# Optimization experiments

Hardware: AMD Instinct MI355X
Metric: run time of the kernel (lower is better)

Reference implementation:

```python
import jax, jax.numpy as jnp
import numpy as np

H, N, M, F, D = 8, 4096, 4096, 1024, 256

def setup_inputs() -> dict:
    key = jax.random.key(0)
    ks = jax.random.split(key, 8)
    sc = 0.02
    return {
        "this": jax.random.normal(ks[0], (N, F), dtype=jnp.float32),
        "that": jax.random.normal(ks[1], (M, F), dtype=jnp.float32),
        "mask": jax.random.randint(ks[2], (N, M), 0, 2) > 0,
        "Wq": jax.random.normal(ks[3], (H, F, D), dtype=jnp.float32) * sc,
        "bq": jnp.zeros((H, D), dtype=jnp.float32),
        "Wk": jax.random.normal(ks[4], (H, F, D), dtype=jnp.float32) * sc,
        "bk": jnp.zeros((H, D), dtype=jnp.float32),
        "Wv": jax.random.normal(ks[5], (H, F, D), dtype=jnp.float32) * sc,
        "bv": jnp.zeros((H, D), dtype=jnp.float32),
        "Wo": jax.random.normal(ks[6], (2 * F, F), dtype=jnp.float32) * sc,
        "bo": jnp.zeros((F,), dtype=jnp.float32),
    }

def reference(this, that, mask, Wq, bq, Wk, bk, Wv, bv, Wo, bo):
    # Per-head projections, batched over heads. q:[h,n,d] k,v:[h,m,d]
    q = jnp.einsum('nf,hfd->hnd', this, Wq) + bq[:, None, :]
    k = jnp.einsum('mf,hfd->hmd', that, Wk) + bk[:, None, :]
    v = jnp.einsum('mf,hfd->hmd', that, Wv) + bv[:, None, :]
    # Unscaled attention scores [h,n,m]
    s = jnp.einsum('hnd,hmd->hnm', q, k)
    neg = 1e9 * (~mask).astype(s.dtype)              # additive mask [n,m]
    head_ids = jnp.arange(s.shape[0])[:, None, None]  # mask applies to heads >= 4 only
    s = jnp.where(head_ids >= 4, s - neg, s)
    w = jax.nn.softmax(s, axis=-1)
    r = jnp.einsum('hnm,hmd->hnd', w, v)              # [h,n,d]
    # concat heads along feature axis in head order -> [n, h*d]
    cat = jnp.transpose(r, (1, 0, 2)).reshape(this.shape[0], -1)
    out = cat @ Wo + bo
    return out + this
```

## Files before the change

kernel.cpp:

```cpp
#include <hip/hip_runtime.h>
#include <stdint.h>


#define H_ 8
#define N_ 4096
#define M_ 4096
#define F_ 1024
#define D_ 256

typedef unsigned short u16;
typedef unsigned int u32;
typedef unsigned long long u64;
typedef unsigned char u8;
typedef __bf16 bf16x8 __attribute__((ext_vector_type(8)));
typedef float f32x4 __attribute__((ext_vector_type(4)));
typedef float f32x16 __attribute__((ext_vector_type(16)));

static __device__ __forceinline__ u16 f2bf(float f) {
  union { float f; u32 u; } v; v.f = f;
  u32 u = v.u + 0x7fffu + ((v.u >> 16) & 1u);
  return (u16)(u >> 16);
}

static __device__ __forceinline__ u32 cvtpk(float lo, float hi) {
  u32 r;
  asm("v_cvt_pk_bf16_f32 %0, %1, %2" : "=v"(r) : "v"(lo), "v"(hi));
  return r;
}

static __device__ __forceinline__ void gld16(const void* g, void* l) {
  __builtin_amdgcn_global_load_lds(
      (const __attribute__((address_space(1))) void*)g,
      (__attribute__((address_space(3))) void*)l, 16, 0, 0);
}

__global__ void k_mask_detect(const u32* __restrict__ m, u32* __restrict__ flag) {
  u32 bad = 0;
  for (int i = threadIdx.x; i < 4096; i += 64) bad |= (m[i] & ~1u);
  u64 anyBad = __ballot(bad != 0);
  if (threadIdx.x == 0) *flag = (anyBad != 0) ? 1u : 0u;
}

__global__ void k_mask_pack2(const void* __restrict__ mp, const u32* __restrict__ flag,
                             u32* __restrict__ out) {
  const int lane = threadIdx.x & 63, wave = threadIdx.x >> 6;
  const int wid = blockIdx.x * 4 + wave;
  const int qrow = wid >> 6;
  const int m0 = (wid & 63) * 64;
  int x;
  if (*flag) x = ((const u8*)mp)[(size_t)qrow * M_ + m0 + lane];
  else       x = ((const int*)mp)[(size_t)qrow * M_ + m0 + lane];
  u64 bits = __ballot(x != 0);
  if (lane == 0) {
    out[(size_t)(m0 >> 5) * N_ + qrow] = (u32)bits;
    out[(size_t)((m0 >> 5) + 1) * N_ + qrow] = (u32)(bits >> 32);
  }
}

__global__ void k_f32_to_bf16(const float* __restrict__ in, u16* __restrict__ out, int n4) {
  int i = blockIdx.x * blockDim.x + threadIdx.x;
  if (i >= n4) return;
  float4 v = ((const float4*)in)[i];
  u32 w0 = (u32)f2bf(v.x) | ((u32)f2bf(v.y) << 16);
  u32 w1 = (u32)f2bf(v.z) | ((u32)f2bf(v.w) << 16);
  ((uint2*)out)[i] = make_uint2(w0, w1);
}

__global__ void k_transpose_f32_bf16(const float* __restrict__ in, u16* __restrict__ out,
                                     int R, int C) {
  __shared__ float t[32][33];
  const int b = blockIdx.z;
  const float* src = in + (size_t)b * R * C;
  u16* dst = out + (size_t)b * R * C;
  const int r0 = blockIdx.x * 32, c0 = blockIdx.y * 32;
  const int tr = threadIdx.x >> 3, tc = (threadIdx.x & 7) * 4;
  float4 v = *(const float4*)(src + (size_t)(r0 + tr) * C + c0 + tc);
  t[tr][tc + 0] = v.x; t[tr][tc + 1] = v.y; t[tr][tc + 2] = v.z; t[tr][tc + 3] = v.w;
  __syncthreads();
  u16* d4 = dst + (size_t)(c0 + tr) * R + r0 + tc;
  d4[0] = f2bf(t[tc + 0][tr]); d4[1] = f2bf(t[tc + 1][tr]);
  d4[2] = f2bf(t[tc + 2][tr]); d4[3] = f2bf(t[tc + 3][tr]);
}

template <int EPI>
__global__ __launch_bounds__(256, 2) void k_gemm_nt(
    const u16* __restrict__ A, const u16* __restrict__ B,
    const float* __restrict__ bias, const float* __restrict__ resid,
    u16* __restrict__ Cb, float* __restrict__ Cf,
    int K, int lda, int ldb, int ldc,
    size_t aBatch, size_t bBatch, size_t biasBatch, size_t cBatch)
{
  __shared__ u16 la[2][128 * 64];
  __shared__ u16 lb[2][128 * 64];
  const int tid = threadIdx.x;
  const int lane = tid & 63, wave = tid >> 6;
  const int g = lane >> 4, fr = lane & 15;
  const int wr = wave >> 1, wc = wave & 1;
  const int z = blockIdx.z;
  const size_t row0 = (size_t)blockIdx.x * 128, col0 = (size_t)blockIdx.y * 128;
  const u16* Ab = A + z * aBatch + row0 * lda;
  const u16* Bb = B + z * bBatch + col0 * ldb;

  f32x4 zero = {0.f, 0.f, 0.f, 0.f};
  f32x4 acc[4][4];
#pragma unroll
  for (int m = 0; m < 4; ++m)
#pragma unroll
    for (int n = 0; n < 4; ++n) acc[m][n] = zero;

  auto STAGE = [&](int bs, int k0) {
#pragma unroll
    for (int i = 0; i < 4; ++i) {
      int c = i * 256 + tid;
      int row = c >> 3, slot = c & 7;
      int srcSlot = slot ^ (row & 7);
      gld16(Ab + (size_t)row * lda + k0 + srcSlot * 8, &la[bs][(i * 256 + wave * 64) * 8]);
      gld16(Bb + (size_t)row * ldb + k0 + srcSlot * 8, &lb[bs][(i * 256 + wave * 64) * 8]);
    }
  };

  STAGE(0, 0);
  __syncthreads();
  int cur = 0;
  for (int k0 = 0; k0 < K; k0 += 64) {
    if (k0 + 64 < K) STAGE(cur ^ 1, k0 + 64);
    const char* lac = (const char*)la[cur];
    const char* lbc = (const char*)lb[cur];
#pragma unroll
    for (int kk = 0; kk < 2; ++kk) {
      const int colByte = (kk * 32 + g * 8) * 2;
      bf16x8 af[4], bfr[4];
#pragma unroll
      for (int m = 0; m < 4; ++m) {
        int row = wr * 64 + m * 16 + fr;
        af[m] = *(const bf16x8*)(lac + ((row * 128 + colByte) ^ ((row & 7) << 4)));
      }
#pragma unroll
      for (int n = 0; n < 4; ++n) {
        int row = wc * 64 + n * 16 + fr;
        bfr[n] = *(const bf16x8*)(lbc + ((row * 128 + colByte) ^ ((row & 7) << 4)));
      }
#pragma unroll
      for (int m = 0; m < 4; ++m)
#pragma unroll
        for (int n = 0; n < 4; ++n)
          acc[m][n] = __builtin_amdgcn_mfma_f32_16x16x32_bf16(af[m], bfr[n], acc[m][n], 0, 0, 0);
    }
    __syncthreads();
    cur ^= 1;
  }

#pragma unroll
  for (int n = 0; n < 4; ++n) {
    const int col = wc * 64 + n * 16 + fr;
    const float bv = bias[z * biasBatch + col0 + col];
#pragma unroll
    for (int m = 0; m < 4; ++m) {
#pragma unroll
      for (int r = 0; r < 4; ++r) {
        const int row = wr * 64 + m * 16 + g * 4 + r;
        const float val = acc[m][n][r] + bv;
        const size_t grow = row0 + row, gcol = col0 + col;
        if (EPI == 0) {
          Cb[(size_t)z * cBatch + grow * ldc + gcol] = f2bf(val);
        } else if (EPI == 1) {
          Cb[(size_t)z * (M_ * D_) + (gcol >> 3) * (M_ * 8) + grow * 8 + (gcol & 7)] = f2bf(val);
        } else if (EPI == 2) {
          Cb[(size_t)z * (M_ * D_) + (grow >> 3) * (D_ * 8) + gcol * 8 + (grow & 7)] = f2bf(val);
        } else {
          Cf[grow * ldc + gcol] = val + resid[grow * ldc + gcol];
        }
      }
    }
  }
}

__global__ __launch_bounds__(256, 2) void k_attn2(
    const u16* __restrict__ q, const u16* __restrict__ k2,
    const u16* __restrict__ v2, const u32* __restrict__ mw,
    u16* __restrict__ cat)
{
  __shared__ u16 smem[32768];
  const int tid = threadIdx.x;
  const int lane = tid & 63, wave = tid >> 6;
  const int hi = lane >> 5, col = lane & 31;
  const int h = blockIdx.x & 7;
  const int xt = blockIdx.x >> 3;
  const int n0w = xt * 128 + wave * 32;
  const float L2E = 1.44269504f;

  const u16* kh = k2 + (size_t)h * (M_ * D_);
  const u16* vh = v2 + (size_t)h * (M_ * D_);

  bf16x8 qf[16];
  {
    const u16* qp = q + ((size_t)h * N_ + n0w + col) * D_ + hi * 8;
#pragma unroll
    for (int dc = 0; dc < 16; ++dc) qf[dc] = *(const bf16x8*)(qp + dc * 16);
  }

  f32x16 racc[8];
#pragma unroll
  for (int i = 0; i < 8; ++i)
#pragma unroll
    for (int e = 0; e < 16; ++e) racc[i][e] = 0.f;

  float mrow = -3e38f, lrow = 0.f;
  const bool useMask = (h >= 4);
  const u32* mp = mw + (n0w + col);

  auto STAGE = [&](int bs, int m0) {
    u16* lkb = smem + bs * 16384;
    u16* lvb = lkb + 8192;
#pragma unroll
    for (int i = 0; i < 4; ++i) {
      int c = i * 256 + tid;
      gld16(kh + (size_t)(c >> 5) * (M_ * 8) + (size_t)(m0 + (c & 31)) * 8,
            lkb + (i * 256 + wave * 64) * 8);
      gld16(vh + (size_t)(c >> 8) * (D_ * 8) + (size_t)m0 * 256 + (size_t)(c & 255) * 8,
            lvb + (i * 256 + wave * 64) * 8);
    }
  };

  STAGE(0, 0);
  __syncthreads();
  int cur = 0;

  for (int it = 0; it < M_ / 32; ++it) {
    const int m0 = it * 32;
    if (it + 1 < M_ / 32) STAGE(cur ^ 1, m0 + 32);
    u32 mword = 0xFFFFFFFFu;
    if (useMask) mword = mp[(size_t)(m0 >> 5) * N_];

    const char* lkb = (const char*)smem + cur * 32768;
    const char* lvb = lkb + 16384;

    f32x16 sA, sB;
#pragma unroll
    for (int e = 0; e < 16; ++e) { sA[e] = 0.f; sB[e] = 0.f; }
#pragma unroll
    for (int dc = 0; dc < 16; dc += 2) {
      bf16x8 a0 = *(const bf16x8*)(lkb + dc * 1024 + lane * 16);
      bf16x8 a1 = *(const bf16x8*)(lkb + dc * 1024 + 1024 + lane * 16);
      sA = __builtin_amdgcn_mfma_f32_32x32x16_bf16(a0, qf[dc], sA, 0, 0, 0);
      sB = __builtin_amdgcn_mfma_f32_32x32x16_bf16(a1, qf[dc + 1], sB, 0, 0, 0);
    }
    f32x16 sv = sA + sB;

    if (useMask) {
      u32 mm = mword >> (hi * 4);
#pragma unroll
      for (int r = 0; r < 16; ++r)
        if (!((mm >> ((r & 3) + 8 * (r >> 2))) & 1u)) sv[r] -= 1e9f;
    }

    float pm = sv[0];
#pragma unroll
    for (int r = 1; r < 16; ++r) pm = fmaxf(pm, sv[r]);
    pm = fmaxf(pm, __shfl_xor(pm, 32));

    if (!__all(pm <= mrow + 8.f)) {
      float mnew = fmaxf(mrow, pm);
      float rs = __builtin_exp2f((mrow - mnew) * L2E);
      lrow *= rs;
#pragma unroll
      for (int i = 0; i < 8; ++i)
#pragma unroll
        for (int e = 0; e < 16; ++e) racc[i][e] *= rs;
      mrow = mnew;
    }
    const float mL = mrow * L2E;
    float p[16];
    float ls = 0.f;
#pragma unroll
    for (int r = 0; r < 16; ++r) {
      p[r] = __builtin_exp2f(sv[r] * L2E - mL);
      ls += p[r];
    }
    ls += __shfl_xor(ls, 32);
    lrow += ls;

#pragma unroll
    for (int ks = 0; ks < 2; ++ks) {
      u32 a0 = cvtpk(p[8 * ks + 0], p[8 * ks + 1]);
      u32 a1 = cvtpk(p[8 * ks + 2], p[8 * ks + 3]);
      u32 b0 = cvtpk(p[8 * ks + 4], p[8 * ks + 5]);
      u32 b1 = cvtpk(p[8 * ks + 6], p[8 * ks + 7]);
      u32 sa0 = __shfl_xor(a0, 32), sa1 = __shfl_xor(a1, 32);
      u32 sb0 = __shfl_xor(b0, 32), sb1 = __shfl_xor(b1, 32);
      union { u32 w[4]; bf16x8 v; } bp;
      bp.w[0] = hi ? sb0 : a0;
      bp.w[1] = hi ? sb1 : a1;
      bp.w[2] = hi ? b0 : sa0;
      bp.w[3] = hi ? b1 : sa1;
      const char* lvk = lvb + ks * 8192 + hi * 4096 + col * 16;
#pragma unroll
      for (int ds = 0; ds < 8; ++ds) {
        bf16x8 av = *(const bf16x8*)(lvk + ds * 512);
        racc[ds] = __builtin_amdgcn_mfma_f32_32x32x16_bf16(av, bp.v, racc[ds], 0, 0, 0);
      }
    }
    __syncthreads();
    cur ^= 1;
  }

  char* lt = (char*)smem + wave * 16384;
  const float inv = 1.f / lrow;
#pragma unroll
  for (int ds = 0; ds < 8; ++ds) {
#pragma unroll
    for (int t = 0; t < 8; ++t) {
      int d0 = ds * 32 + (2 * t & 3) + 8 * (t >> 1) + 4 * hi;
      u32 w = cvtpk(racc[ds][2 * t] * inv, racc[ds][2 * t + 1] * inv);
      *(u32*)(lt + ((col * 512 + d0 * 2) ^ ((col & 7) << 4))) = w;
    }
  }
  __syncthreads();
#pragma unroll
  for (int pch = 0; pch < 16; ++pch) {
    int c = pch * 64 + lane;
    int row = c >> 5, ch = c & 31;
    uint4 val = *(const uint4*)(lt + ((row * 512 + ch * 16) ^ ((row & 7) << 4)));
    *(uint4*)(cat + (size_t)(n0w + row) * (H_ * D_) + (size_t)h * D_ + ch * 8) = val;
  }
}

extern "C" void kernel_launch(void* const* d_in, const int* in_sizes, int n_in,
                              void* d_out, int out_size, void* d_ws, size_t ws_size,
                              hipStream_t stream) {
  const float* thisf = (const float*)d_in[0];
  const float* thatf = (const float*)d_in[1];
  const void* maskp = (const void*)d_in[2];
  const float* Wq = (const float*)d_in[3];
  const float* bq = (const float*)d_in[4];
  const float* Wk = (const float*)d_in[5];
  const float* bk = (const float*)d_in[6];
  const float* Wv = (const float*)d_in[7];
  const float* bv = (const float*)d_in[8];
  const float* Wo = (const float*)d_in[9];
  const float* bo = (const float*)d_in[10];
  float* outp = (float*)d_out;

  char* ws = (char*)d_ws;
  size_t o = 0;
  u16* thisb = (u16*)(ws + o); o += (size_t)N_ * F_ * 2;
  u16* thatb = (u16*)(ws + o); o += (size_t)M_ * F_ * 2;
  u16* wqt = (u16*)(ws + o); o += (size_t)H_ * D_ * F_ * 2;
  u16* wkt = (u16*)(ws + o); o += (size_t)H_ * D_ * F_ * 2;
  u16* wvt = (u16*)(ws + o); o += (size_t)H_ * D_ * F_ * 2;
  u16* wot = (u16*)(ws + o); o += (size_t)F_ * 2 * F_ * 2;
  u16* qb  = (u16*)(ws + o); o += (size_t)H_ * N_ * D_ * 2;
  u16* k2  = (u16*)(ws + o); o += (size_t)H_ * M_ * D_ * 2;
  u16* v2  = (u16*)(ws + o); o += (size_t)H_ * M_ * D_ * 2;
  u16* catb = (u16*)(ws + o); o += (size_t)N_ * 2 * F_ * 2;
  u32* mw2 = (u32*)(ws + o); o += (size_t)(M_ / 32) * N_ * 4;
  u32* mflag = (u32*)(ws + o); o += 256;
  (void)ws_size; (void)in_sizes; (void)n_in; (void)out_size;

  k_mask_detect<<<dim3(1), dim3(64), 0, stream>>>((const u32*)maskp, mflag);
  k_mask_pack2<<<dim3(N_ * (M_ / 64) / 4), dim3(256), 0, stream>>>(maskp, mflag, mw2);

  k_f32_to_bf16<<<dim3(N_ * F_ / 4 / 256), dim3(256), 0, stream>>>(thisf, thisb, N_ * F_ / 4);
  k_f32_to_bf16<<<dim3(M_ * F_ / 4 / 256), dim3(256), 0, stream>>>(thatf, thatb, M_ * F_ / 4);
  k_transpose_f32_bf16<<<dim3(F_ / 32, D_ / 32, H_), dim3(256), 0, stream>>>(Wq, wqt, F_, D_);
  k_transpose_f32_bf16<<<dim3(F_ / 32, D_ / 32, H_), dim3(256), 0, stream>>>(Wk, wkt, F_, D_);
  k_transpose_f32_bf16<<<dim3(F_ / 32, D_ / 32, H_), dim3(256), 0, stream>>>(Wv, wvt, F_, D_);
  k_transpose_f32_bf16<<<dim3(2 * F_ / 32, F_ / 32, 1), dim3(256), 0, stream>>>(Wo, wot, 2 * F_, F_);

  k_gemm_nt<0><<<dim3(N_ / 128, D_ / 128, H_), dim3(256), 0, stream>>>(
      thisb, wqt, bq, nullptr, qb, nullptr, F_, F_, F_, D_,
      (size_t)0, (size_t)D_ * F_, (size_t)D_, (size_t)N_ * D_);
  k_gemm_nt<1><<<dim3(M_ / 128, D_ / 128, H_), dim3(256), 0, stream>>>(
      thatb, wkt, bk, nullptr, k2, nullptr, F_, F_, F_, D_,
      (size_t)0, (size_t)D_ * F_, (size_t)D_, (size_t)0);
  k_gemm_nt<2><<<dim3(M_ / 128, D_ / 128, H_), dim3(256), 0, stream>>>(
      thatb, wvt, bv, nullptr, v2, nullptr, F_, F_, F_, D_,
      (size_t)0, (size_t)D_ * F_, (size_t)D_, (size_t)0);

  k_attn2<<<dim3(256), dim3(256), 0, stream>>>(qb, k2, v2, mw2, catb);

  k_gemm_nt<3><<<dim3(N_ / 128, F_ / 128, 1), dim3(256), 0, stream>>>(
      catb, wot, bo, thisf, nullptr, outp, 2 * F_, 2 * F_, 2 * F_, F_,
      (size_t)0, (size_t)0, (size_t)0, (size_t)0);
}
```

Before: 584.8 us.

## Split attention over key range with merge kernel; fuse K and V projections

The attention kernel now splits the 4096 keys into two halves, launching 512 blocks instead of 256. Each block writes fp16 partial outputs plus the running max and sum to workspace, and a new merge kernel combines the halves and writes the concatenated bf16 output. The aim is to fill more of the GPU's compute units, at the cost of extra global memory traffic, a second launch and fp16 rounding of the partial results. The K and V projection GEMMs are also fused into one launch that treats the contiguous wkt/wvt weights as a single 4096-column matrix. That launch picks its bias from bk or bv by column range and scatters each output into its own layout.

```diff
diff --git a/kernel.cpp b/kernel.cpp
--- a/kernel.cpp
+++ b/kernel.cpp
@@ -153,20 +153,29 @@
 #pragma unroll
   for (int n = 0; n < 4; ++n) {
     const int col = wc * 64 + n * 16 + fr;
-    const float bv = bias[z * biasBatch + col0 + col];
+    const size_t gcol = col0 + col;
+    float bvv;
+    if (EPI == 4) bvv = (gcol < 2048) ? bias[gcol] : resid[gcol - 2048];
+    else bvv = bias[z * biasBatch + gcol];
 #pragma unroll
     for (int m = 0; m < 4; ++m) {
 #pragma unroll
       for (int r = 0; r < 4; ++r) {
         const int row = wr * 64 + m * 16 + g * 4 + r;
-        const float val = acc[m][n][r] + bv;
-        const size_t grow = row0 + row, gcol = col0 + col;
+        const float val = acc[m][n][r] + bvv;
+        const size_t grow = row0 + row;
         if (EPI == 0) {
           Cb[(size_t)z * cBatch + grow * ldc + gcol] = f2bf(val);
-        } else if (EPI == 1) {
-          Cb[(size_t)z * (M_ * D_) + (gcol >> 3) * (M_ * 8) + grow * 8 + (gcol & 7)] = f2bf(val);
-        } else if (EPI == 2) {
-          Cb[(size_t)z * (M_ * D_) + (grow >> 3) * (D_ * 8) + gcol * 8 + (grow & 7)] = f2bf(val);
+        } else if (EPI == 4) {
+          if (gcol < 2048) {
+            const int hh = (int)(gcol >> 8), dd = (int)(gcol & 255);
+            Cb[(size_t)hh * (M_ * D_) + (size_t)(dd >> 3) * (M_ * 8) + grow * 8 + (dd & 7)] = f2bf(val);
+          } else {
+            const size_t g2 = gcol - 2048;
+            const int hh = (int)(g2 >> 8), dd = (int)(g2 & 255);
+            Cb[(size_t)H_ * (M_ * D_) + (size_t)hh * (M_ * D_) +
+               (grow >> 3) * (D_ * 8) + (size_t)dd * 8 + (grow & 7)] = f2bf(val);
+          }
         } else {
           Cf[grow * ldc + gcol] = val + resid[grow * ldc + gcol];
         }
@@ -178,14 +187,15 @@
 __global__ __launch_bounds__(256, 2) void k_attn2(
     const u16* __restrict__ q, const u16* __restrict__ k2,
     const u16* __restrict__ v2, const u32* __restrict__ mw,
-    u16* __restrict__ cat)
+    _Float16* __restrict__ pr, float* __restrict__ pml)
 {
   __shared__ u16 smem[32768];
   const int tid = threadIdx.x;
   const int lane = tid & 63, wave = tid >> 6;
   const int hi = lane >> 5, col = lane & 31;
   const int h = blockIdx.x & 7;
-  const int xt = blockIdx.x >> 3;
+  const int xt = (blockIdx.x >> 3) & 31;
+  const int s = blockIdx.x >> 8;
   const int n0w = xt * 128 + wave * 32;
   const float L2E = 1.44269504f;
 
@@ -222,13 +232,14 @@
     }
   };
 
-  STAGE(0, 0);
+  const int it0 = s * 64, it1 = it0 + 64;
+  STAGE(0, it0 * 32);
   __syncthreads();
   int cur = 0;
 
-  for (int it = 0; it < M_ / 32; ++it) {
+  for (int it = it0; it < it1; ++it) {
     const int m0 = it * 32;
-    if (it + 1 < M_ / 32) STAGE(cur ^ 1, m0 + 32);
+    if (it + 1 < it1) STAGE(cur ^ 1, m0 + 32);
     u32 mword = 0xFFFFFFFFu;
     if (useMask) mword = mp[(size_t)(m0 >> 5) * N_];
 
@@ -304,24 +315,54 @@
     cur ^= 1;
   }
 
-  char* lt = (char*)smem + wave * 16384;
+  _Float16* prw = pr + ((size_t)(s * 8 + h) * 128 + xt * 4 + wave) * 8192;
   const float inv = 1.f / lrow;
 #pragma unroll
   for (int ds = 0; ds < 8; ++ds) {
 #pragma unroll
-    for (int t = 0; t < 8; ++t) {
-      int d0 = ds * 32 + (2 * t & 3) + 8 * (t >> 1) + 4 * hi;
-      u32 w = cvtpk(racc[ds][2 * t] * inv, racc[ds][2 * t + 1] * inv);
-      *(u32*)(lt + ((col * 512 + d0 * 2) ^ ((col & 7) << 4))) = w;
-    }
+    for (int e = 0; e < 16; ++e) {
+      const int d = ds * 32 + (e & 3) + 8 * (e >> 2) + 4 * hi;
+      prw[d * 32 + col] = (_Float16)(racc[ds][e] * inv);
+    }
+  }
+  if (hi == 0) {
+    const size_t mb = ((size_t)(s * 8 + h) * N_ + n0w + col) * 2;
+    pml[mb] = mrow; pml[mb + 1] = lrow;
+  }
+}
+
+__global__ __launch_bounds__(256) void k_attn_merge(
+    const _Float16* __restrict__ pr, const float* __restrict__ pml,
+    u16* __restrict__ cat)
+{
+  __shared__ u16 lt[8192];
+  const int t = threadIdx.x, q = t & 31, dg = t >> 5;
+  const int h = blockIdx.x & 7, wi = blockIdx.x >> 3;
+  const int n0 = wi * 32, n = n0 + q;
+  const size_t b0 = ((size_t)h * 128 + wi) * 8192;
+  const size_t b1 = ((size_t)(8 + h) * 128 + wi) * 8192;
+  const size_t i0 = ((size_t)h * N_ + n) * 2;
+  const size_t i1 = ((size_t)(8 + h) * N_ + n) * 2;
+  const float m0 = pml[i0], l0 = pml[i0 + 1];
+  const float m1 = pml[i1], l1 = pml[i1 + 1];
+  const float mm = fmaxf(m0, m1);
+  float w0 = l0 * __builtin_exp2f((m0 - mm) * 1.44269504f);
+  float w1 = l1 * __builtin_exp2f((m1 - mm) * 1.44269504f);
+  const float inv = 1.f / (w0 + w1);
+  w0 *= inv; w1 *= inv;
+#pragma unroll
+  for (int j = 0; j < 32; ++j) {
+    const int d = dg * 32 + j;
+    const float r = (float)pr[b0 + (size_t)d * 32 + q] * w0 +
+                    (float)pr[b1 + (size_t)d * 32 + q] * w1;
+    lt[q * 256 + d] = f2bf(r);
   }
   __syncthreads();
 #pragma unroll
-  for (int pch = 0; pch < 16; ++pch) {
-    int c = pch * 64 + lane;
-    int row = c >> 5, ch = c & 31;
-    uint4 val = *(const uint4*)(lt + ((row * 512 + ch * 16) ^ ((row & 7) << 4)));
-    *(uint4*)(cat + (size_t)(n0w + row) * (H_ * D_) + (size_t)h * D_ + ch * 8) = val;
+  for (int p = 0; p < 4; ++p) {
+    const int c = p * 256 + t, row = c >> 5, ch = c & 31;
+    uint4 val = *(const uint4*)(lt + row * 256 + ch * 8);
+    *(uint4*)(cat + (size_t)(n0 + row) * (H_ * D_) + (size_t)h * D_ + ch * 8) = val;
   }
 }
 
@@ -343,18 +384,20 @@
 
   char* ws = (char*)d_ws;
   size_t o = 0;
+  u16* wot  = (u16*)(ws + o); o += (size_t)2 * F_ * F_ * 2;
+  u16* qb   = (u16*)(ws + o); o += (size_t)H_ * N_ * D_ * 2;
+  u16* k2   = (u16*)(ws + o); o += (size_t)H_ * M_ * D_ * 2;
+  u16* v2   = (u16*)(ws + o); o += (size_t)H_ * M_ * D_ * 2;
+  u16* catb = (u16*)(ws + o); o += (size_t)N_ * 2 * F_ * 2;
+  u32* mw2  = (u32*)(ws + o); o += (size_t)(M_ / 32) * N_ * 4;
+  float* pml = (float*)(ws + o); o += (size_t)2 * H_ * N_ * 2 * 4;
+  u32* mflag = (u32*)(ws + o); o += 256;
   u16* thisb = (u16*)(ws + o); o += (size_t)N_ * F_ * 2;
   u16* thatb = (u16*)(ws + o); o += (size_t)M_ * F_ * 2;
-  u16* wqt = (u16*)(ws + o); o += (size_t)H_ * D_ * F_ * 2;
-  u16* wkt = (u16*)(ws + o); o += (size_t)H_ * D_ * F_ * 2;
-  u16* wvt = (u16*)(ws + o); o += (size_t)H_ * D_ * F_ * 2;
-  u16* wot = (u16*)(ws + o); o += (size_t)F_ * 2 * F_ * 2;
-  u16* qb  = (u16*)(ws + o); o += (size_t)H_ * N_ * D_ * 2;
-  u16* k2  = (u16*)(ws + o); o += (size_t)H_ * M_ * D_ * 2;
-  u16* v2  = (u16*)(ws + o); o += (size_t)H_ * M_ * D_ * 2;
-  u16* catb = (u16*)(ws + o); o += (size_t)N_ * 2 * F_ * 2;
-  u32* mw2 = (u32*)(ws + o); o += (size_t)(M_ / 32) * N_ * 4;
-  u32* mflag = (u32*)(ws + o); o += 256;
+  u16* wqt  = (u16*)(ws + o); o += (size_t)H_ * D_ * F_ * 2;
+  u16* wkt  = (u16*)(ws + o); o += (size_t)H_ * D_ * F_ * 2;
+  u16* wvt  = (u16*)(ws + o); o += (size_t)H_ * D_ * F_ * 2;
+  _Float16* pr = (_Float16*)thisb;
   (void)ws_size; (void)in_sizes; (void)n_in; (void)out_size;
 
   k_mask_detect<<<dim3(1), dim3(64), 0, stream>>>((const u32*)maskp, mflag);
@@ -370,14 +413,13 @@
   k_gemm_nt<0><<<dim3(N_ / 128, D_ / 128, H_), dim3(256), 0, stream>>>(
       thisb, wqt, bq, nullptr, qb, nullptr, F_, F_, F_, D_,
       (size_t)0, (size_t)D_ * F_, (size_t)D_, (size_t)N_ * D_);
-  k_gemm_nt<1><<<dim3(M_ / 128, D_ / 128, H_), dim3(256), 0, stream>>>(
-      thatb, wkt, bk, nullptr, k2, nullptr, F_, F_, F_, D_,
-      (size_t)0, (size_t)D_ * F_, (size_t)D_, (size_t)0);
-  k_gemm_nt<2><<<dim3(M_ / 128, D_ / 128, H_), dim3(256), 0, stream>>>(
-      thatb, wvt, bv, nullptr, v2, nullptr, F_, F_, F_, D_,
-      (size_t)0, (size_t)D_ * F_, (size_t)D_, (size_t)0);
-
-  k_attn2<<<dim3(256), dim3(256), 0, stream>>>(qb, k2, v2, mw2, catb);
+  k_gemm_nt<4><<<dim3(M_ / 128, 4096 / 128, 1), dim3(256), 0, stream>>>(
+      thatb, wkt, bk, bv, k2, nullptr, F_, F_, F_, 0,
+      (size_t)0, (size_t)0, (size_t)0, (size_t)0);
+
+  k_attn2<<<dim3(512), dim3(256), 0, stream>>>(qb, k2, v2, mw2, pr, pml);
+
+  k_attn_merge<<<dim3(1024), dim3(256), 0, stream>>>(pr, pml, catb);
 
   k_gemm_nt<3><<<dim3(N_ / 128, F_ / 128, 1), dim3(256), 0, stream>>>(
       catb, wot, bo, thisf, nullptr, outp, 2 * F_, 2 * F_, 2 * F_, F_,
```

Result: faster. 511.2 us (-12.6%).
